# Kernel tuning notes

Hardware: AMD Instinct MI355X
Metric: run time of the kernel (lower is better)

The kernel has to match this reference:

```python
import jax, jax.numpy as jnp
import numpy as np

N_HEADS = 16


def setup_inputs() -> dict:
    key = jax.random.key(0)
    k_x, k_q, k_k, k_v, k_o = jax.random.split(key, 5)
    N, S, D = 8, 4096, 1024
    scale = 0.02
    return {
        "x": jax.random.normal(k_x, (N, S, D), dtype=jnp.float32),
        "Wq": jax.random.normal(k_q, (D, D), dtype=jnp.float32) * scale,
        "Wk": jax.random.normal(k_k, (D, D), dtype=jnp.float32) * scale,
        "Wv": jax.random.normal(k_v, (D, D), dtype=jnp.float32) * scale,
        "Wo": jax.random.normal(k_o, (D, D), dtype=jnp.float32) * scale,
        "bo": jnp.zeros((D,), dtype=jnp.float32),
    }


def reference(x, Wq, Wk, Wv, Wo, bo):
    N, S, D = x.shape
    H = N_HEADS
    hd = D // H
    # torch nn.Linear: y = x @ W.T (no bias for q/k/v)
    q = (x @ Wq.T).reshape(N, S, H, hd).transpose(0, 2, 1, 3)  # (N, H, S, hd)
    k = (x @ Wk.T).reshape(N, S, H, hd).transpose(0, 2, 1, 3)
    v = (x @ Wv.T).reshape(N, S, H, hd).transpose(0, 2, 1, 3)
    # Faithful to source: labels q/k bind to the HEADS axis of the permuted
    # tensors, h binds to the sequence axis -> attention over heads, shape
    # (N, S, H, H).
    att = jnp.einsum('nqhd,nkhd->nhqk', q, k)
    att = jax.nn.softmax(att / jnp.sqrt(jnp.asarray(hd, x.dtype)), axis=3)
    out = jnp.einsum('nhqk,nkhd->nqhd', att, v).reshape(N, S, D)
    return out @ Wo.T + bo
```

## Files before the change

kernel.cpp:

```cpp
#include <hip/hip_runtime.h>
#include <hip/hip_bf16.h>
#include <stdint.h>

typedef __hip_bfloat16 bf16;
typedef __attribute__((ext_vector_type(8))) short short8;
typedef __attribute__((ext_vector_type(4))) float f32x4;

__device__ __forceinline__ unsigned short f2bf(float f) {
    bf16 h = __float2bfloat16(f);
    union { bf16 h; unsigned short u; } c; c.h = h; return c.u;
}
__device__ __forceinline__ unsigned int pack2(float a, float b) {
    return (unsigned int)f2bf(a) | ((unsigned int)f2bf(b) << 16);
}

__device__ __forceinline__ void gld16(const void* g, void* l) {
    __builtin_amdgcn_global_load_lds(
        (const __attribute__((address_space(1))) void*)g,
        (__attribute__((address_space(3))) void*)l, 16, 0, 0);
}

__global__ __launch_bounds__(256) void cvt_f32_bf16(
    const float* __restrict__ in, unsigned short* __restrict__ out, long n4)
{
    long i = (long)blockIdx.x * 256 + threadIdx.x;
    if (i >= n4) return;
    float4 v = ((const float4*)in)[i];
    ushort4 o;
    o.x = f2bf(v.x); o.y = f2bf(v.y); o.z = f2bf(v.z); o.w = f2bf(v.w);
    ((ushort4*)out)[i] = o;
}

__global__ __launch_bounds__(256) void cvt_w4(
    const float* __restrict__ a, const float* __restrict__ b,
    const float* __restrict__ c, const float* __restrict__ d,
    unsigned short* __restrict__ out)
{
    const float* src = (blockIdx.y == 0) ? a : (blockIdx.y == 1) ? b
                     : (blockIdx.y == 2) ? c : d;
    long i = (long)blockIdx.x * 256 + threadIdx.x;
    float4 v = ((const float4*)src)[i];
    ushort4 o;
    o.x = f2bf(v.x); o.y = f2bf(v.y); o.z = f2bf(v.z); o.w = f2bf(v.w);
    ((ushort4*)(out + (size_t)blockIdx.y * 1048576))[i] = o;
}


__device__ __forceinline__ void store_c(bf16* C, size_t idx, float v) {
    C[idx] = __float2bfloat16(v);
}
__device__ __forceinline__ void store_c(float* C, size_t idx, float v) {
    C[idx] = v;
}

template <typename CT>
__device__ __forceinline__ void gemm_body256(
    const bf16* __restrict__ A, const bf16* __restrict__ B,
    CT* __restrict__ C, const float* __restrict__ bias,
    int M, int N, int K)
{
    __shared__ char smem[131072];

    const int t    = threadIdx.x;
    const int lane = t & 63;
    const int wave = t >> 6;
    const int wm   = wave >> 2;
    const int wn   = wave & 3;
    const int l16  = lane & 15;
    const int quad = lane >> 4;

    const int gy   = M >> 8;
    const int nwg  = (N >> 8) * gy;
    const int orig = blockIdx.x;
    const int wg   = (orig & 7) * (nwg >> 3) + (orig >> 3);
    const int bx   = wg / gy;
    const int by   = wg - bx * gy;

    const int rowBase = by << 8;
    const int colBase = bx << 8;

    int offA[4], offB[4];
#pragma unroll
    for (int r = 0; r < 4; ++r) {
        int i   = (r << 9) + t;
        int row = i >> 3;
        int sw  = ((i & 7) << 4) ^ ((row & 7) << 4);
        offA[r] = (rowBase + row) * K + (sw >> 1);
        offB[r] = (colBase + row) * K + (sw >> 1);
    }
    const int ldsBase = t << 4;

    auto stage = [&](int bufsel, int k0) {
        char* bA_ = smem + (bufsel << 16);
        char* bB_ = bA_ + 32768;
#pragma unroll
        for (int r = 0; r < 4; ++r) {
            gld16(A + offA[r] + k0, bA_ + ldsBase + (r << 13));
            gld16(B + offB[r] + k0, bB_ + ldsBase + (r << 13));
        }
    };

    f32x4 acc[8][4];
#pragma unroll
    for (int i = 0; i < 8; ++i)
#pragma unroll
        for (int j = 0; j < 4; ++j) acc[i][j] = (f32x4){0.f, 0.f, 0.f, 0.f};

    const int xr    = (l16 & 7) << 4;
    const int kq0   = ((quad << 4)) ^ xr;
    const int kq1   = (64 + (quad << 4)) ^ xr;
    const int aRowB = ((wm << 7) + l16) << 7;
    const int bRowB = ((wn << 6) + l16) << 7;

    auto rdA = [&](short8* dst, char* sA, int mtbase, int kq) {
#pragma unroll
        for (int m = 0; m < 4; ++m)
            dst[m] = *(const short8*)(sA + aRowB + (mtbase + m) * 2048 + kq);
    };
    auto rdB = [&](short8* dst, char* sB, int kq) {
#pragma unroll
        for (int n = 0; n < 4; ++n)
            dst[n] = *(const short8*)(sB + bRowB + n * 2048 + kq);
    };
    auto cluster = [&](const short8* af, const short8* bfr, int mtbase) {
        __builtin_amdgcn_sched_barrier(0);
        __builtin_amdgcn_s_setprio(1);
#pragma unroll
        for (int m = 0; m < 4; ++m)
#pragma unroll
            for (int n = 0; n < 4; ++n)
                acc[mtbase + m][n] = __builtin_amdgcn_mfma_f32_16x16x32_bf16(
                    af[m], bfr[n], acc[mtbase + m][n], 0, 0, 0);
        __builtin_amdgcn_s_setprio(0);
    };

    stage(0, 0);
    stage(1, 64);
    asm volatile("s_waitcnt vmcnt(8)" ::: "memory");
    __builtin_amdgcn_s_barrier();

    short8 A0[4], A1[4], B0[4], B1[4];
    rdA(A0, smem, 0, kq0);
    rdB(B0, smem + 32768, kq0);

    const int ntiles = K >> 6;
    int cur = 0;
    for (int tt = 0; tt < ntiles; ++tt) {
        char* sA = smem + (cur << 16);
        char* sB = sA + 32768;

        rdA(A1, sA, 4, kq0);
        cluster(A0, B0, 0);
        rdA(A0, sA, 0, kq1);
        rdB(B1, sB, kq1);
        cluster(A1, B0, 4);
        rdA(A1, sA, 4, kq1);
        cluster(A0, B1, 0);

        asm volatile("s_waitcnt lgkmcnt(0)" ::: "memory");
        __builtin_amdgcn_sched_barrier(0);
        if (tt + 1 < ntiles) {
            __builtin_amdgcn_s_barrier();
            if (tt + 2 < ntiles) {
                stage(cur, (tt + 2) << 6);
                asm volatile("s_waitcnt vmcnt(8)" ::: "memory");
            } else {
                asm volatile("s_waitcnt vmcnt(0)" ::: "memory");
            }
            __builtin_amdgcn_s_barrier();
            char* nA = smem + ((cur ^ 1) << 16);
            rdA(A0, nA, 0, kq0);
            rdB(B0, nA + 32768, kq0);
        }
        cluster(A1, B1, 4);
        cur ^= 1;
    }

#pragma unroll
    for (int nt2 = 0; nt2 < 4; ++nt2) {
        int col = colBase + (wn << 6) + (nt2 << 4) + l16;
        float bv = bias ? bias[col] : 0.f;
#pragma unroll
        for (int mt = 0; mt < 8; ++mt) {
            int row0 = rowBase + (wm << 7) + (mt << 4) + (quad << 2);
#pragma unroll
            for (int r = 0; r < 4; ++r)
                store_c(C, (size_t)(row0 + r) * N + col, acc[mt][nt2][r] + bv);
        }
    }
}

__global__ __launch_bounds__(512, 2) void gemm_qkv(
    const bf16* __restrict__ A, const bf16* __restrict__ B,
    bf16* __restrict__ C, int M, int N, int K)
{
    gemm_body256<bf16>(A, B, C, nullptr, M, N, K);
}

__global__ __launch_bounds__(512, 2) void gemm_proj(
    const bf16* __restrict__ A, const bf16* __restrict__ B,
    float* __restrict__ C, const float* __restrict__ bias,
    int M, int N, int K)
{
    gemm_body256<float>(A, B, C, bias, M, N, K);
}

__global__ __launch_bounds__(256) void attn_heads(
    const bf16* __restrict__ QKV, bf16* __restrict__ Y)
{
    __shared__ char smem[4 * 3264];
    const int t    = threadIdx.x;
    const int lane = t & 63;
    const int wave = t >> 6;
    const int l16  = lane & 15;
    const int quad = lane >> 4;

    char* Vp = smem + wave * 3264;
    char* Pp = smem + wave * 3264 + 2240;

    const long pos = (long)blockIdx.x * 4 + wave;
    const int  n   = (int)(pos >> 12);
    const int  s   = (int)(pos & 4095);
    const bf16* base = QKV + pos * 3072;

    uint4 v0 = *(const uint4*)(base + 2048 + lane * 8);
    uint4 v1 = *(const uint4*)(base + 2560 + lane * 8);
    short8 qa0 = *(const short8*)(base +        l16 * 64 + quad * 8);
    short8 qa1 = *(const short8*)(base +        l16 * 64 + quad * 8 + 32);
    short8 kb0 = *(const short8*)(base + 1024 + l16 * 64 + quad * 8);
    short8 kb1 = *(const short8*)(base + 1024 + l16 * 64 + quad * 8 + 32);

    {
        int kh0 = lane >> 3, c = lane & 7;
        *(uint4*)(Vp + kh0 * 136 + c * 16) = v0;
        *(uint4*)(Vp + (kh0 + 8) * 136 + c * 16) = v1;
    }

    *(f32x4*)(Pp + lane * 16) = (f32x4){0.f, 0.f, 0.f, 0.f};

    f32x4 sacc = (f32x4){0.f, 0.f, 0.f, 0.f};
    sacc = __builtin_amdgcn_mfma_f32_16x16x32_bf16(qa0, kb0, sacc, 0, 0, 0);
    sacc = __builtin_amdgcn_mfma_f32_16x16x32_bf16(qa1, kb1, sacc, 0, 0, 0);

    float e[4], sm[4];
#pragma unroll
    for (int r = 0; r < 4; r++) { e[r] = __expf(sacc[r] * 0.125f); sm[r] = e[r]; }
#pragma unroll
    for (int m = 1; m <= 8; m <<= 1) {
#pragma unroll
        for (int r = 0; r < 4; r++) sm[r] += __shfl_xor(sm[r], m);
    }
#pragma unroll
    for (int r = 0; r < 4; r++) {
        float p = e[r] * __builtin_amdgcn_rcpf(sm[r]);
        *(unsigned short*)(Pp + (quad * 4 + r) * 64 + l16 * 2) = f2bf(p);
    }

    short8 pfrag = *(const short8*)(Pp + l16 * 64 + quad * 16);

    const char* gbase = Vp + (quad & 1) * (8 * 136)
                           + ((l16 >> 3) * 16) + ((l16 & 7) * 2);
    const size_t yb = ((size_t)n * 4096 + (size_t)(s >> 4)) * 1024
                    + (size_t)(s & 15) * 64;
#pragma unroll
    for (int f = 0; f < 4; f++) {
        short8 vfrag;
#pragma unroll
        for (int j = 0; j < 8; j++)
            vfrag[j] = *(const short*)(gbase + f * 32 + j * 136);
        f32x4 oc = __builtin_amdgcn_mfma_f32_16x16x32_bf16(
            vfrag, pfrag, (f32x4){0.f, 0.f, 0.f, 0.f}, 0, 0, 0);
        uint2 w;
        w.x = pack2(oc[0], oc[1]);
        w.y = pack2(oc[2], oc[3]);
        *(uint2*)(Y + yb + (size_t)l16 * 262144 + 16 * f + quad * 4) = w;
    }
}

extern "C" void kernel_launch(void* const* d_in, const int* in_sizes, int n_in,
                              void* d_out, int out_size, void* d_ws, size_t ws_size,
                              hipStream_t stream) {
    const float* x  = (const float*)d_in[0];
    const float* Wq = (const float*)d_in[1];
    const float* Wk = (const float*)d_in[2];
    const float* Wv = (const float*)d_in[3];
    const float* Wo = (const float*)d_in[4];
    const float* bo = (const float*)d_in[5];
    float* out = (float*)d_out;

    const int M = 8 * 4096;
    const size_t MN = (size_t)M * 1024;

    bf16* Qkv  = (bf16*)d_ws;
    bf16* Xb   = Qkv + (size_t)M * 3072;
    bf16* Yb   = Xb;
    bf16* Wcat = Xb + MN;
    bf16* Wob  = Wcat + (size_t)3072 * 1024;

    {
        long n4 = (long)MN / 4;
        cvt_f32_bf16<<<dim3((unsigned)(n4 / 256)), dim3(256), 0, stream>>>(
            x, (unsigned short*)Xb, n4);
        cvt_w4<<<dim3(1024, 4), dim3(256), 0, stream>>>(
            Wq, Wk, Wv, Wo, (unsigned short*)Wcat);
    }

    dim3 block(512);
    gemm_qkv<<<dim3((3072 / 256) * (M / 256)), block, 0, stream>>>(
        Xb, Wcat, Qkv, M, 3072, 1024);
    attn_heads<<<dim3(M / 4), dim3(256), 0, stream>>>(Qkv, Yb);
    gemm_proj<<<dim3((1024 / 256) * (M / 256)), block, 0, stream>>>(
        Yb, Wob, out, bo, M, 1024, 1024);
}
```

Measured before the change: 591.8 us.

## Restructure GEMM main loop into half-K sub-tiles with finer-grained staged prefetch

Splits each 64-wide K tile into two 32-wide sub-tiles with a new LDS layout and swizzle, and issues global-to-LDS loads for A and B separately, interleaved with the MFMA clusters. The aim is to overlap memory traffic with compute at finer granularity and cut LDS bank conflicts through the new swizzle. The cost is many more workgroup barriers per K tile (eight instead of two) and more complex vmcnt bookkeeping, which could stall waves.

Result: slower. 621.5 us (+5.0%).

```diff
diff --git a/kernel.cpp b/kernel.cpp
--- a/kernel.cpp
+++ b/kernel.cpp
@@ -53,6 +53,10 @@
     C[idx] = v;
 }
 
+#define BAR()   __builtin_amdgcn_s_barrier()
+#define LGKM0() asm volatile("s_waitcnt lgkmcnt(0)" ::: "memory")
+#define VM(n)   asm volatile("s_waitcnt vmcnt(" #n ")" ::: "memory")
+
 template <typename CT>
 __device__ __forceinline__ void gemm_body256(
     const bf16* __restrict__ A, const bf16* __restrict__ B,
@@ -79,25 +83,20 @@
     const int rowBase = by << 8;
     const int colBase = bx << 8;
 
-    int offA[4], offB[4];
-#pragma unroll
-    for (int r = 0; r < 4; ++r) {
-        int i   = (r << 9) + t;
-        int row = i >> 3;
-        int sw  = ((i & 7) << 4) ^ ((row & 7) << 4);
-        offA[r] = (rowBase + row) * K + (sw >> 1);
-        offB[r] = (colBase + row) * K + (sw >> 1);
-    }
-    const int ldsBase = t << 4;
-
-    auto stage = [&](int bufsel, int k0) {
-        char* bA_ = smem + (bufsel << 16);
-        char* bB_ = bA_ + 32768;
-#pragma unroll
-        for (int r = 0; r < 4; ++r) {
-            gld16(A + offA[r] + k0, bA_ + ldsBase + (r << 13));
-            gld16(B + offB[r] + k0, bB_ + ldsBase + (r << 13));
-        }
+    const int cElem = (((t & 3) ^ ((t >> 3) & 3)) << 3);
+    const size_t gA0 = (size_t)(rowBase + (t >> 2)) * K + cElem;
+    const size_t gA1 = (size_t)(rowBase + 128 + (t >> 2)) * K + cElem;
+    const size_t gB0 = (size_t)(colBase + (t >> 2)) * K + cElem;
+    const size_t gB1 = (size_t)(colBase + 128 + (t >> 2)) * K + cElem;
+    const int ldsT = t << 4;
+
+    auto stageA = [&](int kOff, char* region) {
+        gld16(A + gA0 + kOff, region + ldsT);
+        gld16(A + gA1 + kOff, region + 8192 + ldsT);
+    };
+    auto stageB = [&](int kOff, char* region) {
+        gld16(B + gB0 + kOff, region + ldsT);
+        gld16(B + gB1 + kOff, region + 8192 + ldsT);
     };
 
     f32x4 acc[8][4];
@@ -106,24 +105,21 @@
 #pragma unroll
         for (int j = 0; j < 4; ++j) acc[i][j] = (f32x4){0.f, 0.f, 0.f, 0.f};
 
-    const int xr    = (l16 & 7) << 4;
-    const int kq0   = ((quad << 4)) ^ xr;
-    const int kq1   = (64 + (quad << 4)) ^ xr;
-    const int aRowB = ((wm << 7) + l16) << 7;
-    const int bRowB = ((wn << 6) + l16) << 7;
-
-    auto rdA = [&](short8* dst, char* sA, int mtbase, int kq) {
+    const int sx = (quad ^ ((l16 >> 1) & 3)) << 4;
+    const int aoff = ((wm * 64 + (l16 >> 1)) << 7) + ((l16 & 1) << 6) + sx;
+    const int boff = ((wn * 32 + (l16 >> 1)) << 7) + ((l16 & 1) << 6) + sx;
+
+    auto rdA4 = [&](short8* dst, const char* region, int mtbase) {
 #pragma unroll
         for (int m = 0; m < 4; ++m)
-            dst[m] = *(const short8*)(sA + aRowB + (mtbase + m) * 2048 + kq);
-    };
-    auto rdB = [&](short8* dst, char* sB, int kq) {
+            dst[m] = *(const short8*)(region + aoff + (mtbase + m) * 1024);
+    };
+    auto rdB4 = [&](short8* dst, const char* region) {
 #pragma unroll
         for (int n = 0; n < 4; ++n)
-            dst[n] = *(const short8*)(sB + bRowB + n * 2048 + kq);
-    };
-    auto cluster = [&](const short8* af, const short8* bfr, int mtbase) {
-        __builtin_amdgcn_sched_barrier(0);
+            dst[n] = *(const short8*)(region + boff + n * 1024);
+    };
+    auto mm16 = [&](const short8* af, const short8* bfr, int mtbase) {
         __builtin_amdgcn_s_setprio(1);
 #pragma unroll
         for (int m = 0; m < 4; ++m)
@@ -134,46 +130,58 @@
         __builtin_amdgcn_s_setprio(0);
     };
 
-    stage(0, 0);
-    stage(1, 64);
-    asm volatile("s_waitcnt vmcnt(8)" ::: "memory");
-    __builtin_amdgcn_s_barrier();
-
-    short8 A0[4], A1[4], B0[4], B1[4];
-    rdA(A0, smem, 0, kq0);
-    rdB(B0, smem + 32768, kq0);
-
-    const int ntiles = K >> 6;
-    int cur = 0;
-    for (int tt = 0; tt < ntiles; ++tt) {
-        char* sA = smem + (cur << 16);
-        char* sB = sA + 32768;
-
-        rdA(A1, sA, 4, kq0);
-        cluster(A0, B0, 0);
-        rdA(A0, sA, 0, kq1);
-        rdB(B1, sB, kq1);
-        cluster(A1, B0, 4);
-        rdA(A1, sA, 4, kq1);
-        cluster(A0, B1, 0);
-
-        asm volatile("s_waitcnt lgkmcnt(0)" ::: "memory");
-        __builtin_amdgcn_sched_barrier(0);
-        if (tt + 1 < ntiles) {
-            __builtin_amdgcn_s_barrier();
-            if (tt + 2 < ntiles) {
-                stage(cur, (tt + 2) << 6);
-                asm volatile("s_waitcnt vmcnt(8)" ::: "memory");
-            } else {
-                asm volatile("s_waitcnt vmcnt(0)" ::: "memory");
-            }
-            __builtin_amdgcn_s_barrier();
-            char* nA = smem + ((cur ^ 1) << 16);
-            rdA(A0, nA, 0, kq0);
-            rdB(B0, nA + 32768, kq0);
-        }
-        cluster(A1, B1, 4);
-        cur ^= 1;
+    char* slot0 = smem;
+    char* slot1 = smem + 65536;
+
+    stageA(0,  slot0);
+    stageB(0,  slot0 + 32768);
+    stageA(32, slot0 + 16384);
+    stageB(32, slot0 + 49152);
+    stageA(64, slot1);
+    stageB(64, slot1 + 32768);
+    VM(8);
+    BAR();
+
+    const int nt = K >> 6;
+    short8 Alo[4], Ahi[4], Bk[4];
+
+    for (int u = 0; u < nt; ++u) {
+        char* slotC = smem + ((u & 1) << 16);
+        char* slotN = smem + (((u + 1) & 1) << 16);
+        const int kc = u << 6;
+
+        rdB4(Bk, slotC + 32768);
+        rdA4(Alo, slotC, 0);
+        if (u + 1 < nt) stageA(kc + 96, slotN + 16384);
+        BAR();
+        LGKM0();
+        mm16(Alo, Bk, 0);
+        BAR();
+
+        rdA4(Ahi, slotC, 4);
+        if (u + 1 < nt) stageB(kc + 96, slotN + 49152);
+        BAR();
+        LGKM0();
+        mm16(Ahi, Bk, 4);
+        if (u + 1 < nt) { VM(8); } else { VM(0); }
+        BAR();
+
+        rdB4(Bk, slotC + 49152);
+        rdA4(Alo, slotC + 16384, 0);
+        if (u + 2 < nt) stageA(kc + 128, slotC);
+        BAR();
+        LGKM0();
+        mm16(Alo, Bk, 0);
+        BAR();
+
+        rdA4(Ahi, slotC + 16384, 4);
+        if (u + 2 < nt) stageB(kc + 128, slotC + 32768);
+        BAR();
+        LGKM0();
+        mm16(Ahi, Bk, 4);
+        if (u + 2 < nt)      { VM(8); }
+        else if (u + 1 < nt) { VM(4); }
+        BAR();
     }
 
 #pragma unroll
```

## Stage attention output in LDS for coalesced stores and reorder GEMM tile mapping

Applied to the files above, without the earlier changes.

The attention kernel now handles 16 sequence positions per block, four per wave. It writes the per-head outputs into a swizzled shared-memory tile and then flushes full 16-byte coalesced rows to Y, replacing the scattered 8-byte global stores. V is stored transposed in LDS so its fragment loads become vector loads. The GEMM workgroup mapping also changes from column-major to row-major tile order, which alters L2 reuse. The cost is more LDS use per block and a block-wide barrier.

New measurement: 592.5 us. Within noise of the previous version (+0.1%).

```diff
diff --git a/kernel.cpp b/kernel.cpp
--- a/kernel.cpp
+++ b/kernel.cpp
@@ -4,6 +4,7 @@
 
 typedef __hip_bfloat16 bf16;
 typedef __attribute__((ext_vector_type(8))) short short8;
+typedef __attribute__((ext_vector_type(8))) unsigned short ushort8;
 typedef __attribute__((ext_vector_type(4))) float f32x4;
 
 __device__ __forceinline__ unsigned short f2bf(float f) {
@@ -69,12 +70,12 @@
     const int l16  = lane & 15;
     const int quad = lane >> 4;
 
-    const int gy   = M >> 8;
-    const int nwg  = (N >> 8) * gy;
+    const int gx   = N >> 8;
+    const int nwg  = gx * (M >> 8);
     const int orig = blockIdx.x;
     const int wg   = (orig & 7) * (nwg >> 3) + (orig >> 3);
-    const int bx   = wg / gy;
-    const int by   = wg - bx * gy;
+    const int by   = wg / gx;
+    const int bx   = wg - by * gx;
 
     const int rowBase = by << 8;
     const int colBase = bx << 8;
@@ -208,72 +209,95 @@
 __global__ __launch_bounds__(256) void attn_heads(
     const bf16* __restrict__ QKV, bf16* __restrict__ Y)
 {
-    __shared__ char smem[4 * 3264];
+    __shared__ char smem[32768 + 4 * 3584];
     const int t    = threadIdx.x;
     const int lane = t & 63;
     const int wave = t >> 6;
     const int l16  = lane & 15;
     const int quad = lane >> 4;
 
-    char* Vp = smem + wave * 3264;
-    char* Pp = smem + wave * 3264 + 2240;
-
-    const long pos = (long)blockIdx.x * 4 + wave;
-    const int  n   = (int)(pos >> 12);
-    const int  s   = (int)(pos & 4095);
-    const bf16* base = QKV + pos * 3072;
-
-    uint4 v0 = *(const uint4*)(base + 2048 + lane * 8);
-    uint4 v1 = *(const uint4*)(base + 2560 + lane * 8);
-    short8 qa0 = *(const short8*)(base +        l16 * 64 + quad * 8);
-    short8 qa1 = *(const short8*)(base +        l16 * 64 + quad * 8 + 32);
-    short8 kb0 = *(const short8*)(base + 1024 + l16 * 64 + quad * 8);
-    short8 kb1 = *(const short8*)(base + 1024 + l16 * 64 + quad * 8 + 32);
-
-    {
-        int kh0 = lane >> 3, c = lane & 7;
-        *(uint4*)(Vp + kh0 * 136 + c * 16) = v0;
-        *(uint4*)(Vp + (kh0 + 8) * 136 + c * 16) = v1;
-    }
+    char* Ys = smem;
+    char* Vt = smem + 32768 + wave * 3584;
+    char* Pp = Vt + 2560;
+
+    const int pos16 = blockIdx.x << 4;
+    const int n = pos16 >> 12;
+    const int g = (pos16 & 4095) >> 4;
 
     *(f32x4*)(Pp + lane * 16) = (f32x4){0.f, 0.f, 0.f, 0.f};
 
-    f32x4 sacc = (f32x4){0.f, 0.f, 0.f, 0.f};
-    sacc = __builtin_amdgcn_mfma_f32_16x16x32_bf16(qa0, kb0, sacc, 0, 0, 0);
-    sacc = __builtin_amdgcn_mfma_f32_16x16x32_bf16(qa1, kb1, sacc, 0, 0, 0);
-
-    float e[4], sm[4];
-#pragma unroll
-    for (int r = 0; r < 4; r++) { e[r] = __expf(sacc[r] * 0.125f); sm[r] = e[r]; }
-#pragma unroll
-    for (int m = 1; m <= 8; m <<= 1) {
-#pragma unroll
-        for (int r = 0; r < 4; r++) sm[r] += __shfl_xor(sm[r], m);
-    }
-#pragma unroll
-    for (int r = 0; r < 4; r++) {
-        float p = e[r] * __builtin_amdgcn_rcpf(sm[r]);
-        *(unsigned short*)(Pp + (quad * 4 + r) * 64 + l16 * 2) = f2bf(p);
-    }
-
-    short8 pfrag = *(const short8*)(Pp + l16 * 64 + quad * 16);
-
-    const char* gbase = Vp + (quad & 1) * (8 * 136)
-                           + ((l16 >> 3) * 16) + ((l16 & 7) * 2);
-    const size_t yb = ((size_t)n * 4096 + (size_t)(s >> 4)) * 1024
-                    + (size_t)(s & 15) * 64;
-#pragma unroll
-    for (int f = 0; f < 4; f++) {
-        short8 vfrag;
-#pragma unroll
-        for (int j = 0; j < 8; j++)
-            vfrag[j] = *(const short*)(gbase + f * 32 + j * 136);
-        f32x4 oc = __builtin_amdgcn_mfma_f32_16x16x32_bf16(
-            vfrag, pfrag, (f32x4){0.f, 0.f, 0.f, 0.f}, 0, 0, 0);
-        uint2 w;
-        w.x = pack2(oc[0], oc[1]);
-        w.y = pack2(oc[2], oc[3]);
-        *(uint2*)(Y + yb + (size_t)l16 * 262144 + 16 * f + quad * 4) = w;
+#pragma unroll 2
+    for (int p = 0; p < 4; ++p) {
+        const int sidx = (wave << 2) + p;
+        const bf16* base = QKV + (size_t)(pos16 + sidx) * 3072;
+
+        ushort8 v0 = *(const ushort8*)(base + 2048 + lane * 8);
+        ushort8 v1 = *(const ushort8*)(base + 2560 + lane * 8);
+        short8 qa0 = *(const short8*)(base +        l16 * 64 + quad * 8);
+        short8 qa1 = *(const short8*)(base +        l16 * 64 + quad * 8 + 32);
+        short8 kb0 = *(const short8*)(base + 1024 + l16 * 64 + quad * 8);
+        short8 kb1 = *(const short8*)(base + 1024 + l16 * 64 + quad * 8 + 32);
+
+        {
+            const int dbase = (lane & 7) << 3;
+            const int kcol  = (lane >> 3) << 1;
+#pragma unroll
+            for (int e = 0; e < 8; ++e) {
+                *(unsigned short*)(Vt + (dbase + e) * 40 + kcol)      = v0[e];
+                *(unsigned short*)(Vt + (dbase + e) * 40 + 16 + kcol) = v1[e];
+            }
+        }
+
+        f32x4 sacc = (f32x4){0.f, 0.f, 0.f, 0.f};
+        sacc = __builtin_amdgcn_mfma_f32_16x16x32_bf16(qa0, kb0, sacc, 0, 0, 0);
+        sacc = __builtin_amdgcn_mfma_f32_16x16x32_bf16(qa1, kb1, sacc, 0, 0, 0);
+
+        float e[4], sm[4];
+#pragma unroll
+        for (int r = 0; r < 4; r++) { e[r] = __expf(sacc[r] * 0.125f); sm[r] = e[r]; }
+#pragma unroll
+        for (int m = 1; m <= 8; m <<= 1) {
+#pragma unroll
+            for (int r = 0; r < 4; r++) sm[r] += __shfl_xor(sm[r], m);
+        }
+#pragma unroll
+        for (int r = 0; r < 4; r++) {
+            float pv = e[r] * __builtin_amdgcn_rcpf(sm[r]);
+            *(unsigned short*)(Pp + (quad * 4 + r) * 64 + l16 * 2) = f2bf(pv);
+        }
+
+        short8 pfrag = *(const short8*)(Pp + l16 * 64 + quad * 16);
+
+        const char* gb = Vt + l16 * 40 + ((quad & 1) << 4);
+        const int ybase  = l16 << 11;
+        const int cBase0 = sidx << 3;
+#pragma unroll
+        for (int f = 0; f < 4; ++f) {
+            union { uint2 a2[2]; short8 s; } vf;
+            vf.a2[0] = *(const uint2*)(gb + f * 640);
+            vf.a2[1] = *(const uint2*)(gb + f * 640 + 8);
+            f32x4 oc = __builtin_amdgcn_mfma_f32_16x16x32_bf16(
+                vf.s, pfrag, (f32x4){0.f, 0.f, 0.f, 0.f}, 0, 0, 0);
+            uint2 w;
+            w.x = pack2(oc[0], oc[1]);
+            w.y = pack2(oc[2], oc[3]);
+            int c  = cBase0 + (f << 1) + (quad >> 1);
+            int cp = c ^ ((c >> 3) & 7) ^ (l16 & 7);
+            *(uint2*)(Ys + ybase + (cp << 4) + ((quad & 1) << 3)) = w;
+        }
+    }
+
+    __syncthreads();
+
+    const size_t rowB = (size_t)n * 4096 + (size_t)g;
+#pragma unroll
+    for (int i = 0; i < 8; ++i) {
+        int j  = (i << 8) + t;
+        int qh = j >> 7;
+        int c  = j & 127;
+        int cp = c ^ ((c >> 3) & 7) ^ (qh & 7);
+        uint4 v = *(const uint4*)(Ys + (qh << 11) + (cp << 4));
+        *(uint4*)(Y + ((rowB + (size_t)qh * 256) << 10) + (c << 3)) = v;
     }
 }
 
@@ -308,7 +332,7 @@
     dim3 block(512);
     gemm_qkv<<<dim3((3072 / 256) * (M / 256)), block, 0, stream>>>(
         Xb, Wcat, Qkv, M, 3072, 1024);
-    attn_heads<<<dim3(M / 4), dim3(256), 0, stream>>>(Qkv, Yb);
+    attn_heads<<<dim3(M / 16), dim3(256), 0, stream>>>(Qkv, Yb);
     gemm_proj<<<dim3((1024 / 256) * (M / 256)), block, 0, stream>>>(
         Yb, Wob, out, bo, M, 1024, 1024);
 }
```
